# Optimization experiments

Hardware: AMD Instinct MI355X
Metric: run time of the kernel (lower is better)

The kernel has to match this reference:

```python
import jax, jax.numpy as jnp
import numpy as np

N = 50000      # nodes
E = 800000     # edges (avg degree 16)
IN = 128       # input feature dim
D = 128        # embed dim (heads=1, concat)
SLOPE = 0.2    # GATv2Conv default negative_slope


def setup_inputs() -> dict:
    key = jax.random.key(0)
    ks = jax.random.split(key, 16)
    s_in = 1.0 / np.sqrt(IN)
    s_d = 1.0 / np.sqrt(D)
    inp = {
        "node_fts": jax.random.normal(ks[0], (N, IN), dtype=jnp.float32),
        "edge_index": jax.random.randint(ks[1], (2, E), 0, N, dtype=jnp.int64),
        # layer 1 (in_dim -> embed_dim)
        "Wl1": jax.random.normal(ks[2], (IN, D), dtype=jnp.float32) * s_in,
        "bl1": jnp.zeros((D,), dtype=jnp.float32),
        "Wr1": jax.random.normal(ks[3], (IN, D), dtype=jnp.float32) * s_in,
        "br1": jnp.zeros((D,), dtype=jnp.float32),
        "att1": jax.random.normal(ks[4], (D,), dtype=jnp.float32) * s_d,
        "bias1": jnp.zeros((D,), dtype=jnp.float32),
        # layer 2 (embed_dim -> embed_dim)
        "Wl2": jax.random.normal(ks[5], (D, D), dtype=jnp.float32) * s_d,
        "bl2": jnp.zeros((D,), dtype=jnp.float32),
        "Wr2": jax.random.normal(ks[6], (D, D), dtype=jnp.float32) * s_d,
        "br2": jnp.zeros((D,), dtype=jnp.float32),
        "att2": jax.random.normal(ks[7], (D,), dtype=jnp.float32) * s_d,
        "bias2": jnp.zeros((D,), dtype=jnp.float32),
    }
    return inp


def gatv2_layer(x, src, dst, Wl, bl, Wr, br, att, bias):
    # GATv2Conv (heads=1, share_weights=False):
    #   x_j (source message features) = lin_l(x), x_i (target) = lin_r(x)
    xl = x @ Wl + bl                                      # [N, D]
    xr = x @ Wr + br                                      # [N, D]
    e = jax.nn.leaky_relu(xl[src] + xr[dst], SLOPE)       # [E, D]
    logits = e @ att                                      # [E]
    # softmax over incoming edges of each target node
    m = jax.ops.segment_max(logits, dst, num_segments=N)  # [N], -inf for isolated
    m = jnp.where(jnp.isneginf(m), 0.0, m)
    a = jnp.exp(logits - m[dst])                          # [E]
    s = jax.ops.segment_sum(a, dst, num_segments=N)       # [N]
    a = a / jnp.maximum(s[dst], 1e-16)
    out = jax.ops.segment_sum(a[:, None] * xl[src], dst, num_segments=N)  # [N, D]
    return out + bias


def reference(node_fts, edge_index,
              Wl1, bl1, Wr1, br1, att1, bias1,
              Wl2, bl2, Wr2, br2, att2, bias2):
    src, dst = edge_index[0], edge_index[1]
    x = jax.nn.relu(gatv2_layer(node_fts, src, dst, Wl1, bl1, Wr1, br1, att1, bias1))
    x = jax.nn.relu(gatv2_layer(x, src, dst, Wl2, bl2, Wr2, br2, att2, bias2))
    return x
```

## Files before the change

kernel.cpp:

```cpp
#include <hip/hip_runtime.h>
#include <hip/hip_bf16.h>
#include <hip/hip_fp16.h>

#define N_NODES 50000
#define N_EDGES 800000
#define DIM 128
#define NGROUPS (N_NODES / 16)
#define LROW2 132
#define KBUCKET 196
#define BCAP 5120
#define EPB 2000

typedef __attribute__((ext_vector_type(8))) _Float16 hfrag8;
typedef __attribute__((ext_vector_type(4))) float f32x4;
typedef _Float16 h2 __attribute__((ext_vector_type(2)));

__device__ __forceinline__ h2 u2h(uint u){ union{uint u; h2 h;} c; c.u = u; return c.h; }

__device__ __forceinline__ float rowsum16(float p) {
  union { float f; int i; } a, b;
  a.f = p;
  b.i = __builtin_amdgcn_update_dpp(0, a.i, 0x128, 0xF, 0xF, true); a.f += b.f;
  b.i = __builtin_amdgcn_update_dpp(0, a.i, 0x124, 0xF, 0xF, true); a.f += b.f;
  b.i = __builtin_amdgcn_update_dpp(0, a.i, 0x122, 0xF, 0xF, true); a.f += b.f;
  b.i = __builtin_amdgcn_update_dpp(0, a.i, 0x121, 0xF, 0xF, true); a.f += b.f;
  return a.f;
}


__global__ __launch_bounds__(256) void bucket_scatter_k(
    const int* __restrict__ src, const int* __restrict__ dst,
    int* __restrict__ bucket_cnt, uint* __restrict__ bucketdata)
{
  __shared__ int cnt[KBUCKET], base[KBUCKET], cur[KBUCKET];
  int tid = threadIdx.x;
  for (int t = tid; t < KBUCKET; t += 256) { cnt[t] = 0; cur[t] = 0; }
  __syncthreads();
  int e0 = blockIdx.x * EPB;
  int dreg[8];
  #pragma unroll
  for (int it = 0; it < 8; it++) {
    int i = it*256 + tid;
    dreg[it] = (i < EPB) ? dst[e0 + i] : -1;
    if (i < EPB) atomicAdd(&cnt[dreg[it] >> 8], 1);
  }
  __syncthreads();
  for (int t = tid; t < KBUCKET; t += 256)
    base[t] = atomicAdd(&bucket_cnt[t], cnt[t]);
  __syncthreads();
  #pragma unroll
  for (int it = 0; it < 8; it++) {
    int i = it*256 + tid;
    if (i < EPB) {
      int s = src[e0 + i], d = dreg[it];
      int b = d >> 8;
      int r = atomicAdd(&cur[b], 1);
      bucketdata[(size_t)b * BCAP + base[b] + r] = ((uint)s << 8) | (uint)(d & 255);
    }
  }
}

__global__ __launch_bounds__(64) void prep_w(
    const float* __restrict__ Wl1, const float* __restrict__ Wr1,
    const float* __restrict__ Wl2, const float* __restrict__ Wr2,
    _Float16* __restrict__ wb, int* __restrict__ bucket_cnt)
{
  int bid = blockIdx.x;
  if (bid == 0) {
    for (int t = threadIdx.x; t < KBUCKET; t += 64) bucket_cnt[t] = 0;
  }
  int layer = bid >> 6, rest = bid & 63;
  int C = rest >> 4, g = rest & 15;
  int lane = threadIdx.x;
  int m = lane & 15, q = lane >> 4;
  int dim = g*16 + m;
  const float* W = layer ? (dim < 128 ? Wl2 : Wr2) : (dim < 128 ? Wl1 : Wr1);
  int dcol = dim & 127;
  _Float16 h[8];
  #pragma unroll
  for (int j = 0; j < 8; j++) {
    int k = C*32 + q*8 + j;
    h[j] = (_Float16)W[(size_t)k*DIM + dcol];
  }
  size_t off = ((size_t)bid*64 + lane)*8;
  *(hfrag8*)(wb + off) = *(hfrag8*)h;
}

__global__ __launch_bounds__(256) void gemm1_csr_k(
    const float* __restrict__ x, const _Float16* __restrict__ wb,
    const float* __restrict__ bl, const float* __restrict__ br,
    __half* __restrict__ xlh, __half* __restrict__ xrh,
    const int* __restrict__ bucket_cnt, const uint* __restrict__ bucketdata,
    int* __restrict__ row_start, int* __restrict__ csr_soff)
{
  __shared__ float lds[4][16*LROW2];
  __shared__ int hist[256], cur[256];
  __shared__ int wsumA[4], wsumB[4];
  int tid = threadIdx.x;

  if (blockIdx.x < KBUCKET) {
    int b = blockIdx.x;
    int lane = tid & 63, w = tid >> 6;
    int vv = (tid < b) ? bucket_cnt[tid] : 0;
    #pragma unroll
    for (int off = 32; off > 0; off >>= 1) vv += __shfl_xor(vv, off, 64);
    if (lane == 0) wsumA[w] = vv;
    hist[tid] = 0;
    __syncthreads();
    int base_csr = wsumA[0] + wsumA[1] + wsumA[2] + wsumA[3];
    int cnt = bucket_cnt[b];
    int node0 = b << 8;
    const uint* bd = bucketdata + (size_t)b * BCAP;
    for (int i = tid; i < cnt; i += 256)
      atomicAdd(&hist[bd[i] & 255], 1);
    __syncthreads();
    int v = hist[tid];
    int inc = v;
    #pragma unroll
    for (int off = 1; off < 64; off <<= 1) {
      int y = __shfl_up(inc, off, 64);
      if (lane >= off) inc += y;
    }
    if (lane == 63) wsumB[w] = inc;
    __syncthreads();
    int wpre = 0;
    #pragma unroll
    for (int i = 0; i < 4; i++) if (i < w) wpre += wsumB[i];
    int excl = wpre + inc - v;
    int node = node0 + tid;
    if (node < N_NODES) row_start[node] = base_csr + excl;
    if (b == 0 && tid == 0) row_start[N_NODES] = N_EDGES;
    cur[tid] = excl;
    __syncthreads();
    for (int i = tid; i < cnt; i += 256) {
      uint p = bd[i];
      int r = atomicAdd(&cur[p & 255], 1);
      csr_soff[base_csr + r] = (int)(p & 0xFFFFFF00u);
    }
    return;
  }

  int wv = tid >> 6, lane = tid & 63;
  int G = (blockIdx.x - KBUCKET) * 4 + wv;
  if (G >= NGROUPS) return;

  int m = lane & 15, q = lane >> 4;
  const float* xrow = x + (size_t)(G*16 + m)*DIM + q*8;

  f32x4 acc[16];
  #pragma unroll
  for (int g = 0; g < 16; g++) acc[g] = (f32x4)(0.f);

  #pragma unroll 1
  for (int C = 0; C < 4; C++) {
    float v[8];
    *(float4*)(v)     = *(const float4*)(xrow + C*32);
    *(float4*)(v + 4) = *(const float4*)(xrow + C*32 + 4);
    _Float16 hh[8];
    #pragma unroll
    for (int j = 0; j < 8; j++) hh[j] = (_Float16)v[j];
    hfrag8 ah = *(hfrag8*)hh;
    #pragma unroll
    for (int g = 0; g < 16; g++) {
      size_t boff = ((size_t)(C*16 + g)*64 + lane)*8;
      hfrag8 bh = *(const hfrag8*)(wb + boff);
      acc[g] = __builtin_amdgcn_mfma_f32_16x16x32_f16(ah, bh, acc[g], 0, 0, 0);
    }
  }

  float* wlds = lds[wv];
  int dcol = (lane & 31) * 4;
  int rowsel = lane >> 5;
  #pragma unroll
  for (int half = 0; half < 2; half++) {
    #pragma unroll
    for (int g = 0; g < 8; g++) {
      #pragma unroll
      for (int r = 0; r < 4; r++)
        wlds[(q*4 + r)*LROW2 + g*16 + m] = acc[half*8 + g][r];
    }
    const float* B = half ? br : bl;
    ushort* outh = half ? (ushort*)xrh : (ushort*)xlh;
    float4 bv = *(const float4*)(B + dcol);
    #pragma unroll
    for (int it = 0; it < 8; it++) {
      int i = it*2 + rowsel;
      float4 vv2 = *(const float4*)(wlds + i*LROW2 + dcol);
      int node = G*16 + i;
      __half2 h0 = __floats2half2_rn(vv2.x + bv.x, vv2.y + bv.y);
      __half2 h1 = __floats2half2_rn(vv2.z + bv.z, vv2.w + bv.w);
      uint2 pk = make_uint2(*(uint*)&h0, *(uint*)&h1);
      *(uint2*)(outh + (size_t)node*DIM + dcol) = pk;
    }
  }
}


#define GAT_LDI4(OFF, RBASE)                                            \
  _Pragma("unroll")                                                     \
  for (int j = 0; j < 4; j++) OFF[j] = csr_soff[(RBASE) + j];

#define GAT_LDR4(OFF, RAW)                                              \
  _Pragma("unroll")                                                     \
  for (int j = 0; j < 4; j++)                                           \
    RAW[j] = *(const uint4*)(xb + (size_t)(uint)OFF[j]);

#define GAT_BODY(RAW, WEXPR)                                            \
  _Pragma("unroll")                                                     \
  for (int j = 0; j < 4; j++) {                                         \
    h2 v01 = u2h(RAW[j].x), v23 = u2h(RAW[j].y);                        \
    h2 v45 = u2h(RAW[j].z), v67 = u2h(RAW[j].w);                        \
    h2 s01 = v01 + xr01, s23 = v23 + xr23;                              \
    h2 s45 = v45 + xr45, s67 = v67 + xr67;                              \
    s01 = __builtin_elementwise_max(s01, s01 * c02);                    \
    s23 = __builtin_elementwise_max(s23, s23 * c02);                    \
    s45 = __builtin_elementwise_max(s45, s45 * c02);                    \
    s67 = __builtin_elementwise_max(s67, s67 * c02);                    \
    float pA = __builtin_amdgcn_fdot2(s01, a01, 0.f, false);            \
    pA = __builtin_amdgcn_fdot2(s23, a23, pA, false);                   \
    float pB = __builtin_amdgcn_fdot2(s45, a45, 0.f, false);            \
    pB = __builtin_amdgcn_fdot2(s67, a67, pB, false);                   \
    float p = rowsum16(pA + pB);                                        \
    float w = (WEXPR);                                                  \
    l += w;                                                             \
    b0a = fmaf(w, (float)v01.x, b0a); b1a = fmaf(w, (float)v01.y, b1a); \
    b2a = fmaf(w, (float)v23.x, b2a); b3a = fmaf(w, (float)v23.y, b3a); \
    b4a = fmaf(w, (float)v45.x, b4a); b5a = fmaf(w, (float)v45.y, b5a); \
    b6a = fmaf(w, (float)v67.x, b6a); b7a = fmaf(w, (float)v67.y, b7a); \
  }

__device__ __forceinline__ void gather_core(
    int node, int hl,
    const __half* __restrict__ xlh, const __half* __restrict__ xrh,
    const int* __restrict__ row_start, const int* __restrict__ csr_soff,
    const float* __restrict__ att, const float* __restrict__ bias,
    float4& o0, float4& o1)
{
  int r0 = row_start[node];
  int deg = row_start[node + 1] - r0;

  uint4 rx = *(const uint4*)((const ushort*)xrh + (size_t)node*DIM + hl*8);
  h2 xr01 = u2h(rx.x), xr23 = u2h(rx.y), xr45 = u2h(rx.z), xr67 = u2h(rx.w);
  const float* ap = att + hl*8;
  float4 af0 = *(const float4*)(ap);
  float4 af1 = *(const float4*)(ap + 4);
  const float L2E = 1.44269504088896f;
  h2 a01 = {(_Float16)(af0.x*L2E), (_Float16)(af0.y*L2E)};
  h2 a23 = {(_Float16)(af0.z*L2E), (_Float16)(af0.w*L2E)};
  h2 a45 = {(_Float16)(af1.x*L2E), (_Float16)(af1.y*L2E)};
  h2 a67 = {(_Float16)(af1.z*L2E), (_Float16)(af1.w*L2E)};
  const h2 c02 = {(_Float16)0.2f, (_Float16)0.2f};

  float l = 0.f;
  float b0a=0,b1a=0,b2a=0,b3a=0,b4a=0,b5a=0,b6a=0,b7a=0;
  const char* xb = (const char*)xlh + hl*16;

  int offA[4]; uint4 rawA[4];
  int offB[4]; uint4 rawB[4];
  int nfull = deg & ~3;

  if (nfull > 0) { GAT_LDI4(offA, r0); GAT_LDR4(offA, rawA); }
  #pragma unroll 1
  for (int t = 0; t < nfull; t += 8) {
    bool hasB = (t + 4 < nfull);
    if (hasB) { GAT_LDI4(offB, r0 + t + 4); GAT_LDR4(offB, rawB); }
    GAT_BODY(rawA, exp2f(p));
    if (t + 8 < nfull) { GAT_LDI4(offA, r0 + t + 8); GAT_LDR4(offA, rawA); }
    if (hasB) GAT_BODY(rawB, exp2f(p));
  }
  int rem = deg - nfull;
  if (rem > 0) {
    #pragma unroll
    for (int j = 0; j < 4; j++) {
      int rr = r0 + nfull + (j < rem ? j : rem - 1);
      offA[j] = csr_soff[rr];
    }
    GAT_LDR4(offA, rawA);
    GAT_BODY(rawA, (j < rem) ? exp2f(p) : 0.f);
  }

  float inv = 1.f / fmaxf(l, 1e-16f);
  const float* bp = bias + hl*8;
  float4 c0 = *(const float4*)(bp);
  float4 c1 = *(const float4*)(bp + 4);
  o0.x = fmaxf(fmaf(b0a, inv, c0.x), 0.f);
  o0.y = fmaxf(fmaf(b1a, inv, c0.y), 0.f);
  o0.z = fmaxf(fmaf(b2a, inv, c0.z), 0.f);
  o0.w = fmaxf(fmaf(b3a, inv, c0.w), 0.f);
  o1.x = fmaxf(fmaf(b4a, inv, c1.x), 0.f);
  o1.y = fmaxf(fmaf(b5a, inv, c1.y), 0.f);
  o1.z = fmaxf(fmaf(b6a, inv, c1.z), 0.f);
  o1.w = fmaxf(fmaf(b7a, inv, c1.w), 0.f);
}

__global__ __launch_bounds__(64, 4) void fused_g1_gemm2_k(
    const __half* __restrict__ xlh, const __half* __restrict__ xrh,
    const int* __restrict__ row_start, const int* __restrict__ csr_soff,
    const float* __restrict__ att, const float* __restrict__ bias,
    const _Float16* __restrict__ wb2,
    const float* __restrict__ bl2, const float* __restrict__ br2,
    __half* __restrict__ xlh2, __half* __restrict__ xrh2)
{
  __shared__ ushort xs[16*132];
  int lane = threadIdx.x;
  int q4 = lane >> 4, hl = lane & 15;
  int base = blockIdx.x * 16;

  #pragma unroll 1
  for (int rr = 0; rr < 4; rr++) {
    int nl = rr*4 + q4;
    float4 o0, o1;
    gather_core(base + nl, hl, xlh, xrh, row_start, csr_soff, att, bias, o0, o1);
    __half2 p0 = __floats2half2_rn(o0.x, o0.y);
    __half2 p1 = __floats2half2_rn(o0.z, o0.w);
    __half2 p2 = __floats2half2_rn(o1.x, o1.y);
    __half2 p3 = __floats2half2_rn(o1.z, o1.w);
    uint4 pk = make_uint4(*(uint*)&p0, *(uint*)&p1, *(uint*)&p2, *(uint*)&p3);
    *(uint4*)((char*)xs + nl*264 + ((hl*16) ^ ((nl&7)<<4))) = pk;
  }

  hfrag8 ah[4];
  #pragma unroll
  for (int C = 0; C < 4; C++)
    ah[C] = *(const hfrag8*)((const char*)xs + hl*264 +
                             ((C*64 + q4*16) ^ ((hl&7)<<4)));

  #pragma unroll 1
  for (int half = 0; half < 2; half++) {
    f32x4 acc[8];
    #pragma unroll
    for (int g = 0; g < 8; g++) acc[g] = (f32x4)(0.f);
    #pragma unroll
    for (int C = 0; C < 4; C++) {
      #pragma unroll
      for (int g = 0; g < 8; g++) {
        int gg = half*8 + g;
        hfrag8 bh = *(const hfrag8*)(wb2 + ((size_t)(C*16 + gg)*64 + lane)*8);
        acc[g] = __builtin_amdgcn_mfma_f32_16x16x32_f16(ah[C], bh, acc[g], 0, 0, 0);
      }
    }
    const float* B = half ? br2 : bl2;
    #pragma unroll
    for (int g = 0; g < 8; g++) {
      float bv = B[g*16 + hl];
      #pragma unroll
      for (int r = 0; r < 4; r++) {
        __half hv = __float2half_rn(acc[g][r] + bv);
        xs[(q4*4 + r)*132 + g*16 + hl] = *(ushort*)&hv;
      }
    }
    __half* dsth = half ? xrh2 : xlh2;
    #pragma unroll
    for (int i = 0; i < 4; i++) {
      int row = i*4 + q4;
      uint4 v = *(const uint4*)((const char*)xs + row*264 + hl*16);
      *(uint4*)((ushort*)dsth + (size_t)(base + row)*DIM + hl*8) = v;
    }
  }
}

__global__ __launch_bounds__(256) void gat_gather2(
    const __half* __restrict__ xlh, const __half* __restrict__ xrh,
    const int* __restrict__ row_start, const int* __restrict__ csr_soff,
    const float* __restrict__ att, const float* __restrict__ bias,
    float* __restrict__ outf)
{
  int wave = (blockIdx.x * 256 + threadIdx.x) >> 6;
  int lane = threadIdx.x & 63;
  int q4 = lane >> 4;
  int hl = lane & 15;
  int node = wave * 4 + q4;
  float4 o0, o1;
  gather_core(node, hl, xlh, xrh, row_start, csr_soff, att, bias, o0, o1);
  float* op = outf + (size_t)node*DIM + hl*8;
  *(float4*)(op)     = o0;
  *(float4*)(op + 4) = o1;
}

extern "C" void kernel_launch(void* const* d_in, const int* in_sizes, int n_in,
                              void* d_out, int out_size, void* d_ws, size_t ws_size,
                              hipStream_t stream)
{
  const float* node_fts = (const float*)d_in[0];
  const int*  edge_index = (const int*)d_in[1];
  const float* Wl1 = (const float*)d_in[2];
  const float* bl1 = (const float*)d_in[3];
  const float* Wr1 = (const float*)d_in[4];
  const float* br1 = (const float*)d_in[5];
  const float* att1 = (const float*)d_in[6];
  const float* bias1 = (const float*)d_in[7];
  const float* Wl2 = (const float*)d_in[8];
  const float* bl2 = (const float*)d_in[9];
  const float* Wr2 = (const float*)d_in[10];
  const float* br2 = (const float*)d_in[11];
  const float* att2 = (const float*)d_in[12];
  const float* bias2 = (const float*)d_in[13];
  const int* src = edge_index;
  const int* dst = edge_index + N_EDGES;

  char* ws = (char*)d_ws;
  __half* xlh = (__half*)ws;               ws += (size_t)N_NODES*DIM*2;
  __half* xrh = (__half*)ws;               ws += (size_t)N_NODES*DIM*2;
  __half* xlh2 = (__half*)ws;              ws += (size_t)N_NODES*DIM*2;
  __half* xrh2 = (__half*)ws;              ws += (size_t)N_NODES*DIM*2;
  _Float16* wb = (_Float16*)ws;            ws += 2*4*16*64*8*2;
  int* row_start   = (int*)ws;             ws += (N_NODES+1)*4;
  int* csr_soff    = (int*)ws;             ws += (size_t)N_EDGES*4;
  int* bucket_cnt  = (int*)ws;             ws += KBUCKET*4;
  uint* bucketdata = (uint*)ws;            ws += (size_t)KBUCKET*BCAP*4;

  const int W_LAYER = 4*16*64*8;

  int gemm_blocks = (NGROUPS + 3) / 4;
  int gather_blocks = N_NODES / 16;

  prep_w<<<128, 64, 0, stream>>>(Wl1, Wr1, Wl2, Wr2, wb, bucket_cnt);
  bucket_scatter_k<<<N_EDGES/EPB, 256, 0, stream>>>(src, dst, bucket_cnt, bucketdata);
  gemm1_csr_k<<<KBUCKET + gemm_blocks, 256, 0, stream>>>(
      node_fts, wb, bl1, br1, xlh, xrh,
      bucket_cnt, bucketdata, row_start, csr_soff);
  fused_g1_gemm2_k<<<NGROUPS, 64, 0, stream>>>(
      xlh, xrh, row_start, csr_soff, att1, bias1,
      wb + W_LAYER, bl2, br2, xlh2, xrh2);
  gat_gather2<<<gather_blocks, 256, 0, stream>>>(
      xlh2, xrh2, row_start, csr_soff, att2, bias2, (float*)d_out);
}
```

Baseline: 228.8 us.

## Spread fused gather+GEMM across four waves and deepen gather prefetch in layer 2

The fused layer-1 gather plus layer-2 GEMM kernel now runs with 256 threads per 16-node block instead of one 64-thread wave. Each wave gathers four nodes in parallel, then computes a quarter of the output columns with MFMA, and all threads write the results through a shared tile. This replaces the earlier serial loop over four node groups, raising parallelism and latency hiding at the cost of two block barriers. The layer-2 gather kernel uses a new templated variant that keeps four 4-edge batches in flight instead of two, which adds register pressure.

Result: faster. 220.6 us (-3.6%).

```diff
diff --git a/kernel.cpp b/kernel.cpp
--- a/kernel.cpp
+++ b/kernel.cpp
@@ -10,6 +10,7 @@
 #define KBUCKET 196
 #define BCAP 5120
 #define EPB 2000
+#define OSTR 260
 
 typedef __attribute__((ext_vector_type(8))) _Float16 hfrag8;
 typedef __attribute__((ext_vector_type(4))) float f32x4;
@@ -229,6 +230,7 @@
     b6a = fmaf(w, (float)v67.x, b6a); b7a = fmaf(w, (float)v67.y, b7a); \
   }
 
+template<int DEEP>
 __device__ __forceinline__ void gather_core(
     int node, int hl,
     const __half* __restrict__ xlh, const __half* __restrict__ xrh,
@@ -259,14 +261,32 @@
   int offB[4]; uint4 rawB[4];
   int nfull = deg & ~3;
 
-  if (nfull > 0) { GAT_LDI4(offA, r0); GAT_LDR4(offA, rawA); }
-  #pragma unroll 1
-  for (int t = 0; t < nfull; t += 8) {
-    bool hasB = (t + 4 < nfull);
-    if (hasB) { GAT_LDI4(offB, r0 + t + 4); GAT_LDR4(offB, rawB); }
-    GAT_BODY(rawA, exp2f(p));
-    if (t + 8 < nfull) { GAT_LDI4(offA, r0 + t + 8); GAT_LDR4(offA, rawA); }
-    if (hasB) GAT_BODY(rawB, exp2f(p));
+  if constexpr (DEEP == 0) {
+    if (nfull > 0) { GAT_LDI4(offA, r0); GAT_LDR4(offA, rawA); }
+    #pragma unroll 1
+    for (int t = 0; t < nfull; t += 8) {
+      bool hasB = (t + 4 < nfull);
+      if (hasB) { GAT_LDI4(offB, r0 + t + 4); GAT_LDR4(offB, rawB); }
+      GAT_BODY(rawA, exp2f(p));
+      if (t + 8 < nfull) { GAT_LDI4(offA, r0 + t + 8); GAT_LDR4(offA, rawA); }
+      if (hasB) GAT_BODY(rawB, exp2f(p));
+    }
+  } else {
+    int offC[4]; uint4 rawC[4];
+    int offD[4]; uint4 rawD[4];
+    if (nfull > 0) { GAT_LDI4(offA, r0);     GAT_LDR4(offA, rawA); }
+    if (nfull > 4) { GAT_LDI4(offB, r0 + 4); GAT_LDR4(offB, rawB); }
+    #pragma unroll 1
+    for (int t = 0; t < nfull; t += 16) {
+      if (t + 8  < nfull) { GAT_LDI4(offC, r0 + t + 8);  GAT_LDR4(offC, rawC); }
+      GAT_BODY(rawA, exp2f(p));
+      if (t + 12 < nfull) { GAT_LDI4(offD, r0 + t + 12); GAT_LDR4(offD, rawD); }
+      if (t + 4  < nfull) GAT_BODY(rawB, exp2f(p));
+      if (t + 16 < nfull) { GAT_LDI4(offA, r0 + t + 16); GAT_LDR4(offA, rawA); }
+      if (t + 8  < nfull) GAT_BODY(rawC, exp2f(p));
+      if (t + 20 < nfull) { GAT_LDI4(offB, r0 + t + 20); GAT_LDR4(offB, rawB); }
+      if (t + 12 < nfull) GAT_BODY(rawD, exp2f(p));
+    }
   }
   int rem = deg - nfull;
   if (rem > 0) {
@@ -293,7 +313,7 @@
   o1.w = fmaxf(fmaf(b7a, inv, c1.w), 0.f);
 }
 
-__global__ __launch_bounds__(64, 4) void fused_g1_gemm2_k(
+__global__ __launch_bounds__(256) void fused_g1_gemm2_k(
     const __half* __restrict__ xlh, const __half* __restrict__ xrh,
     const int* __restrict__ row_start, const int* __restrict__ csr_soff,
     const float* __restrict__ att, const float* __restrict__ bias,
@@ -301,61 +321,62 @@
     const float* __restrict__ bl2, const float* __restrict__ br2,
     __half* __restrict__ xlh2, __half* __restrict__ xrh2)
 {
-  __shared__ ushort xs[16*132];
-  int lane = threadIdx.x;
+  __shared__ ushort xs[16*128];
+  __shared__ ushort outs[16*OSTR];
+  int tid = threadIdx.x;
+  int wv = tid >> 6, lane = tid & 63;
   int q4 = lane >> 4, hl = lane & 15;
+  int nl = wv*4 + q4;
   int base = blockIdx.x * 16;
 
-  #pragma unroll 1
-  for (int rr = 0; rr < 4; rr++) {
-    int nl = rr*4 + q4;
-    float4 o0, o1;
-    gather_core(base + nl, hl, xlh, xrh, row_start, csr_soff, att, bias, o0, o1);
-    __half2 p0 = __floats2half2_rn(o0.x, o0.y);
-    __half2 p1 = __floats2half2_rn(o0.z, o0.w);
-    __half2 p2 = __floats2half2_rn(o1.x, o1.y);
-    __half2 p3 = __floats2half2_rn(o1.z, o1.w);
-    uint4 pk = make_uint4(*(uint*)&p0, *(uint*)&p1, *(uint*)&p2, *(uint*)&p3);
-    *(uint4*)((char*)xs + nl*264 + ((hl*16) ^ ((nl&7)<<4))) = pk;
-  }
-
-  hfrag8 ah[4];
-  #pragma unroll
-  for (int C = 0; C < 4; C++)
-    ah[C] = *(const hfrag8*)((const char*)xs + hl*264 +
-                             ((C*64 + q4*16) ^ ((hl&7)<<4)));
-
-  #pragma unroll 1
-  for (int half = 0; half < 2; half++) {
-    f32x4 acc[8];
-    #pragma unroll
-    for (int g = 0; g < 8; g++) acc[g] = (f32x4)(0.f);
-    #pragma unroll
-    for (int C = 0; C < 4; C++) {
-      #pragma unroll
-      for (int g = 0; g < 8; g++) {
-        int gg = half*8 + g;
-        hfrag8 bh = *(const hfrag8*)(wb2 + ((size_t)(C*16 + gg)*64 + lane)*8);
-        acc[g] = __builtin_amdgcn_mfma_f32_16x16x32_f16(ah[C], bh, acc[g], 0, 0, 0);
-      }
-    }
-    const float* B = half ? br2 : bl2;
-    #pragma unroll
-    for (int g = 0; g < 8; g++) {
-      float bv = B[g*16 + hl];
-      #pragma unroll
-      for (int r = 0; r < 4; r++) {
-        __half hv = __float2half_rn(acc[g][r] + bv);
-        xs[(q4*4 + r)*132 + g*16 + hl] = *(ushort*)&hv;
-      }
-    }
-    __half* dsth = half ? xrh2 : xlh2;
-    #pragma unroll
-    for (int i = 0; i < 4; i++) {
-      int row = i*4 + q4;
-      uint4 v = *(const uint4*)((const char*)xs + row*264 + hl*16);
-      *(uint4*)((ushort*)dsth + (size_t)(base + row)*DIM + hl*8) = v;
-    }
+  float4 o0, o1;
+  gather_core<0>(base + nl, hl, xlh, xrh, row_start, csr_soff, att, bias, o0, o1);
+  __half2 p0 = __floats2half2_rn(o0.x, o0.y);
+  __half2 p1 = __floats2half2_rn(o0.z, o0.w);
+  __half2 p2 = __floats2half2_rn(o1.x, o1.y);
+  __half2 p3 = __floats2half2_rn(o1.z, o1.w);
+  uint4 pk = make_uint4(*(uint*)&p0, *(uint*)&p1, *(uint*)&p2, *(uint*)&p3);
+  *(uint4*)((char*)xs + nl*256 + ((hl*16) ^ ((nl&7)<<4))) = pk;
+  __syncthreads();
+
+  int m = lane & 15, q = lane >> 4;
+  f32x4 acc[4];
+  #pragma unroll
+  for (int g = 0; g < 4; g++) acc[g] = (f32x4)(0.f);
+  #pragma unroll
+  for (int C = 0; C < 4; C++) {
+    hfrag8 ah = *(const hfrag8*)((const char*)xs + m*256 + ((C*64 + q*16) ^ ((m&7)<<4)));
+    #pragma unroll
+    for (int g = 0; g < 4; g++) {
+      int gg = wv*4 + g;
+      size_t boff = ((size_t)(C*16 + gg)*64 + lane)*8;
+      hfrag8 bh = *(const hfrag8*)(wb2 + boff);
+      acc[g] = __builtin_amdgcn_mfma_f32_16x16x32_f16(ah, bh, acc[g], 0, 0, 0);
+    }
+  }
+  #pragma unroll
+  for (int g = 0; g < 4; g++) {
+    int gg = wv*4 + g;
+    int dim = gg*16 + m;
+    float bv = (gg < 8) ? bl2[dim] : br2[dim - 128];
+    #pragma unroll
+    for (int r = 0; r < 4; r++) {
+      int row = q*4 + r;
+      __half hv = __float2half_rn(acc[g][r] + bv);
+      outs[row*OSTR + gg*16 + m] = *(ushort*)&hv;
+    }
+  }
+  __syncthreads();
+  #pragma unroll
+  for (int p = 0; p < 2; p++) {
+    int c = p*256 + tid;
+    int row = c >> 5, off = c & 31;
+    uint4 v = *(const uint4*)((const char*)outs + row*(OSTR*2) + off*16);
+    int nodeo = base + row;
+    int d0 = off*8;
+    ushort* dstp = (d0 < 128) ? ((ushort*)xlh2 + (size_t)nodeo*DIM + d0)
+                              : ((ushort*)xrh2 + (size_t)nodeo*DIM + (d0 - 128));
+    *(uint4*)dstp = v;
   }
 }
 
@@ -371,7 +392,7 @@
   int hl = lane & 15;
   int node = wave * 4 + q4;
   float4 o0, o1;
-  gather_core(node, hl, xlh, xrh, row_start, csr_soff, att, bias, o0, o1);
+  gather_core<1>(node, hl, xlh, xrh, row_start, csr_soff, att, bias, o0, o1);
   float* op = outf + (size_t)node*DIM + hl*8;
   *(float4*)(op)     = o0;
   *(float4*)(op + 4) = o1;
@@ -419,7 +440,7 @@
   gemm1_csr_k<<<KBUCKET + gemm_blocks, 256, 0, stream>>>(
       node_fts, wb, bl1, br1, xlh, xrh,
       bucket_cnt, bucketdata, row_start, csr_soff);
-  fused_g1_gemm2_k<<<NGROUPS, 64, 0, stream>>>(
+  fused_g1_gemm2_k<<<gather_blocks, 256, 0, stream>>>(
       xlh, xrh, row_start, csr_soff, att1, bias1,
       wb + W_LAYER, bl2, br2, xlh2, xrh2);
   gat_gather2<<<gather_blocks, 256, 0, stream>>>(
```
